# Kernel optimization log

Measured on AMD Instinct MI355X. Metric: run time of the kernel, lower is better.

The kernel has to match this reference:

```python
import jax, jax.numpy as jnp
import numpy as np

IN_FEATURES = 1024
OUT_FEATURES = 1024
BATCH = 32
SEQ = 1024
EPS = 1e-8


def setup_inputs() -> dict:
    key = jax.random.key(0)
    k1, k2, k3 = jax.random.split(key, 3)
    Efou = jax.random.normal(k1, (BATCH, SEQ, IN_FEATURES), dtype=jnp.float32)
    y = jax.random.normal(k2, (BATCH, IN_FEATURES), dtype=jnp.float32)
    weight = jax.random.normal(k3, (IN_FEATURES, OUT_FEATURES), dtype=jnp.float32)
    return {"Efou": Efou, "y": y, "weight": weight}


def reference(Efou, y, weight):
    # scale = 1/sqrt(in_features)
    scale = 1.0 / np.sqrt(np.float32(weight.shape[0]))
    ys = y * scale  # (b, i) == per-sample column scaling of weight
    # Demodulation norm: sum_i (scale*W[i,o]*y[b,i])^2 = (ys^2) @ (W^2)
    d = jax.lax.rsqrt(jnp.einsum('bi,io->bo', ys * ys, weight * weight) + EPS)  # (b, o)
    # Efou @ (scale*W*y*d) == ((Efou*ys) @ W) * d  -- same math, avoids (b,i,o) weight
    out = jnp.einsum('bsi,io->bso', Efou * ys[:, None, :], weight) * d[:, None, :]
    return out
```

## Files before the change

kernel.cpp:

```cpp
#include <hip/hip_runtime.h>

#define AS1 __attribute__((address_space(1)))
#define AS3 __attribute__((address_space(3)))

typedef __bf16 bf16x8 __attribute__((ext_vector_type(8)));
typedef float f32x4 __attribute__((ext_vector_type(4)));
typedef unsigned short ushort8 __attribute__((ext_vector_type(8)));

__device__ __forceinline__ unsigned short f2bf(float f) {
  union { float f; unsigned u; } v; v.f = f;
  unsigned u = v.u;
  unsigned r = (u + 0x7fffu + ((u >> 16) & 1u)) >> 16;
  return (unsigned short)r;
}

__global__ __launch_bounds__(256) void dcalc_a_kernel(const float* __restrict__ y,
                                                      const float* __restrict__ W,
                                                      float* __restrict__ partial) {
  __shared__ float ysq[32][32];
  const int o = blockIdx.x * 256 + threadIdx.x;
  const int i0 = blockIdx.y * 32;
  for (int e = threadIdx.x; e < 1024; e += 256) {
    int il = e >> 5, b = e & 31;
    float t = y[b * 1024 + i0 + il] * 0.03125f;
    ysq[il][b] = t * t;
  }
  __syncthreads();

  f32x4 acc[8] = {};
#pragma unroll
  for (int il = 0; il < 32; ++il) {
    float w = W[(size_t)(i0 + il) * 1024 + o];
    float w2 = w * w;
#pragma unroll
    for (int b4 = 0; b4 < 8; ++b4) {
      f32x4 q = *(const f32x4*)&ysq[il][b4 * 4];
#pragma unroll
      for (int k = 0; k < 4; ++k) acc[b4][k] = fmaf(q[k], w2, acc[b4][k]);
    }
  }
  float* p = partial + (size_t)blockIdx.y * 32768 + o;
#pragma unroll
  for (int b4 = 0; b4 < 8; ++b4)
#pragma unroll
    for (int k = 0; k < 4; ++k) p[(b4 * 4 + k) * 1024] = acc[b4][k];
}

__global__ __launch_bounds__(256) void dcalc_b_kernel(const float* __restrict__ partial,
                                                      float* __restrict__ dmod) {
  const int bo = blockIdx.x * 256 + threadIdx.x;
  float acc = 0.f;
#pragma unroll 8
  for (int is = 0; is < 32; ++is) acc += partial[(size_t)is * 32768 + bo];
  dmod[bo] = rsqrtf(acc + 1e-8f);
}

__global__ void wconv_kernel(const float* __restrict__ W,
                             unsigned short* __restrict__ WT) {
  __shared__ float t[32][33];
  const int tx = threadIdx.x;
  const int ty = threadIdx.y;
  const int i0 = blockIdx.y * 32;
  const int o0 = blockIdx.x * 32;
#pragma unroll
  for (int k = 0; k < 4; ++k)
    t[ty + k * 8][tx] = W[(size_t)(i0 + ty + k * 8) * 1024 + o0 + tx];
  __syncthreads();
#pragma unroll
  for (int k = 0; k < 4; ++k)
    WT[(size_t)(o0 + ty + k * 8) * 1024 + i0 + tx] = f2bf(t[tx][ty + k * 8]);
}

#define NT 16
#define LDS_TILE 65536

#define BAR __builtin_amdgcn_s_barrier()
#define LGKM0 asm volatile("s_waitcnt lgkmcnt(0)" ::: "memory")
#define VM(n) asm volatile("s_waitcnt vmcnt(" #n ")" ::: "memory")
#define SCHB __builtin_amdgcn_sched_barrier(0)
#define PRIO(x) __builtin_amdgcn_s_setprio(x)

#define STG_B(r, t, dst)                                                     \
  __builtin_amdgcn_global_load_lds(                                          \
      (const AS1 void*)(Ws + (size_t)(r) * 64 * 2048 + (t) * 128),           \
      (AS3 void*)((dst) + 32768 + (r) * 8192 + sldso), 16, 0, 0)

#define A_ISSUE(t)                                                           \
  {                                                                          \
    const float* asrc = Efou + (size_t)(m0 + argp * 4) * 1024 + (t) * 64 + k8; \
    _Pragma("unroll") for (int rr = 0; rr < 4; ++rr) {                       \
      pa[rr][0] = *(const f32x4*)(asrc + rr * 1024);                         \
      pa[rr][1] = *(const f32x4*)(asrc + rr * 1024 + 4);                     \
    }                                                                        \
    yv[0] = *(const f32x4*)(ysS + (t) * 64 + k8);                            \
    yv[1] = *(const f32x4*)(ysS + (t) * 64 + k8 + 4);                        \
  }

#define A_WRITE(dst)                                                         \
  {                                                                          \
    _Pragma("unroll") for (int rr = 0; rr < 4; ++rr) {                       \
      const int row = argp * 4 + rr;                                         \
      ushort8 ov;                                                            \
      _Pragma("unroll") for (int q = 0; q < 4; ++q) {                        \
        ov[q] = f2bf(pa[rr][0][q] * yv[0][q]);                               \
        ov[q + 4] = f2bf(pa[rr][1][q] * yv[1][q]);                           \
      }                                                                      \
      *(ushort8*)((dst) + row * 128 + ((kslot * 16) ^ ((row & 7) << 4))) = ov; \
    }                                                                        \
  }

#define RD_A(mh, mi, kk)                                                     \
  (*(const bf16x8*)(Ab + (wr * 128 + ((mh) * 4 + (mi)) * 16 + l15) * 128 +   \
                    ((((kk) * 64 + lhi * 16)) ^ swz_rd)))
#define RD_B(nh, ni, kk)                                                     \
  (*(const bf16x8*)(Bb + (wc * 64 + ((nh) * 2 + (ni)) * 16 + l15) * 128 +    \
                    ((((kk) * 64 + lhi * 16)) ^ swz_rd)))

#define LD_A(mh)                                                             \
  { _Pragma("unroll") for (int mi = 0; mi < 4; ++mi)                         \
      _Pragma("unroll") for (int kk = 0; kk < 2; ++kk)                       \
        a[mi][kk] = RD_A(mh, mi, kk); }
#define LD_B(nh)                                                             \
  { _Pragma("unroll") for (int ni = 0; ni < 2; ++ni)                         \
      _Pragma("unroll") for (int kk = 0; kk < 2; ++kk)                       \
        bfr[ni][kk] = RD_B(nh, ni, kk); }

#define MM(mh, nh)                                                           \
  do {                                                                       \
    _Pragma("unroll") for (int mi = 0; mi < 4; ++mi)                         \
      _Pragma("unroll") for (int ni = 0; ni < 2; ++ni)                       \
        _Pragma("unroll") for (int kk = 0; kk < 2; ++kk)                     \
          acc[(mh) * 4 + mi][(nh) * 2 + ni] =                                \
              __builtin_amdgcn_mfma_f32_16x16x32_bf16(                       \
                  a[mi][kk], bfr[ni][kk], acc[(mh) * 4 + mi][(nh) * 2 + ni], \
                  0, 0, 0);                                                  \
  } while (0)

__global__ __launch_bounds__(512, 2) void gemmf_kernel(
    const float* __restrict__ Efou, const float* __restrict__ y,
    const unsigned short* __restrict__ WT, const float* __restrict__ dmod,
    float* __restrict__ out) {
  extern __shared__ char lds[];
  float* ysS = (float*)(lds + 2 * LDS_TILE);

  const int tid = threadIdx.x;
  const int bid = blockIdx.x;
  const int wg = (bid & 7) * 64 + (bid >> 3);
  const int bm = wg >> 2, bn = wg & 3;
  const int m0 = bm * 256, n0 = bn * 256;
  const int b = m0 >> 10;

  const int w = tid >> 6, l = tid & 63;
  const int wr = w >> 2, wc = w & 3;
  const int l15 = l & 15, lhi = l >> 4;
  const int swz_rd = (l15 & 7) << 4;

  const int kslot = tid & 7;
  const int k8 = kslot * 8;
  const int argp = tid >> 3;

  const int srow = tid >> 3;
  const int scb = ((tid & 7) << 4) ^ ((srow & 7) << 4);
  const char* Ws = (const char*)WT + (size_t)(n0 + srow) * 2048 + scb;
  const int sldso = tid * 16;

  f32x4 acc[8][4] = {};
  bf16x8 a[4][2], bfr[2][2];
  f32x4 pa[4][2], yv[2];

  {
    float2 yy = *(const float2*)(y + b * 1024 + tid * 2);
    ysS[2 * tid] = yy.x * 0.03125f;
    ysS[2 * tid + 1] = yy.y * 0.03125f;
  }
  __syncthreads();
  {
    char* d0 = lds;
    STG_B(0, 0, d0); STG_B(1, 0, d0); STG_B(2, 0, d0); STG_B(3, 0, d0);
    A_ISSUE(0);
    A_WRITE(d0);
  }
  VM(0); LGKM0; BAR;

  for (int t = 0; t < NT - 1; ++t) {
    const char* Ab = lds + (t & 1) * LDS_TILE;
    const char* Bb = Ab + 32768;
    char* dN = lds + ((t & 1) ^ 1) * LDS_TILE;
    const int t1 = t + 1;
    LD_A(0); LD_B(0);
    A_ISSUE(t1);
    STG_B(0, t1, dN); STG_B(1, t1, dN);
    BAR; LGKM0; SCHB; PRIO(1); MM(0, 0); PRIO(0); SCHB; BAR;
    LD_B(1);
    STG_B(2, t1, dN); STG_B(3, t1, dN);
    BAR; LGKM0; SCHB; PRIO(1); MM(0, 1); PRIO(0); SCHB; BAR;
    LD_A(1); LD_B(0);
    BAR; LGKM0; SCHB; PRIO(1); MM(1, 0); PRIO(0); SCHB; BAR;
    LD_B(1);
    BAR; LGKM0; SCHB; PRIO(1); MM(1, 1); PRIO(0); SCHB;
    A_WRITE(dN);
    VM(0);
    LGKM0;
    BAR;
  }

  {
    const char* Ab = lds + ((NT - 1) & 1) * LDS_TILE;
    const char* Bb = Ab + 32768;
    LD_A(0); LD_B(0);
    BAR; LGKM0; SCHB; PRIO(1); MM(0, 0); PRIO(0); SCHB; BAR;
    LD_B(1);
    BAR; LGKM0; SCHB; PRIO(1); MM(0, 1); PRIO(0); SCHB; BAR;
    LD_A(1); LD_B(0);
    BAR; LGKM0; SCHB; PRIO(1); MM(1, 0); PRIO(0); SCHB; BAR;
    LD_B(1);
    BAR; LGKM0; SCHB; PRIO(1); MM(1, 1); PRIO(0); SCHB;
  }

  const int col0 = n0 + wc * 64 + l15;
  float dv[4];
#pragma unroll
  for (int nf = 0; nf < 4; ++nf) dv[nf] = dmod[b * 1024 + col0 + nf * 16];
#pragma unroll
  for (int mf = 0; mf < 8; ++mf) {
#pragma unroll
    for (int j = 0; j < 4; ++j) {
      const int row = m0 + wr * 128 + mf * 16 + lhi * 4 + j;
      float* orow = out + (size_t)row * 1024 + col0;
#pragma unroll
      for (int nf = 0; nf < 4; ++nf) orow[nf * 16] = acc[mf][nf][j] * dv[nf];
    }
  }
}

extern "C" void kernel_launch(void* const* d_in, const int* in_sizes, int n_in,
                              void* d_out, int out_size, void* d_ws, size_t ws_size,
                              hipStream_t stream) {
  const float* Efou = (const float*)d_in[0];
  const float* y    = (const float*)d_in[1];
  const float* W    = (const float*)d_in[2];
  float* out = (float*)d_out;

  unsigned short* WT = (unsigned short*)d_ws;
  float* dmod        = (float*)(WT + (size_t)1024 * 1024);
  float* dpart       = dmod + 32768;

  hipFuncSetAttribute((const void*)gemmf_kernel,
                      hipFuncAttributeMaxDynamicSharedMemorySize, 135168);

  dcalc_a_kernel<<<dim3(4, 32), 256, 0, stream>>>(y, W, dpart);
  dcalc_b_kernel<<<128, 256, 0, stream>>>(dpart, dmod);
  wconv_kernel<<<dim3(32, 32), dim3(32, 8), 0, stream>>>(W, WT);
  gemmf_kernel<<<512, 512, 135168, stream>>>(Efou, y, WT, dmod, out);
}
```

Measured before the change: 129.6 us.

## Issue A-tile loads via inline asm and convert-write mid-iteration with partial vmcnt wait

Replaces the compiler-generated fp32 A-tile global loads with inline-asm dwordx4 loads that use an SGPR base and VGPR offsets. It also moves the bf16 convert-and-LDS-write of the next A tile from the end of the iteration to the middle, after a partial vmcnt wait. All four B-stage LDS DMAs are now issued up front. The intent is to overlap the A conversion with the MFMA phases and shorten the serial tail before the barrier. The risk is that the vmcnt counts assume a fixed ordering of outstanding loads, and the LDS write now lands while MFMAs are still reading the other buffer.

Result: no change. 131.4 us (+1.4%).

```diff
diff --git a/kernel.cpp b/kernel.cpp
--- a/kernel.cpp
+++ b/kernel.cpp
@@ -85,18 +85,27 @@
       (const AS1 void*)(Ws + (size_t)(r) * 64 * 2048 + (t) * 128),           \
       (AS3 void*)((dst) + 32768 + (r) * 8192 + sldso), 16, 0, 0)
 
-#define A_ISSUE(t)                                                           \
+#define AISS(t1)                                                             \
   {                                                                          \
-    const float* asrc = Efou + (size_t)(m0 + argp * 4) * 1024 + (t) * 64 + k8; \
-    _Pragma("unroll") for (int rr = 0; rr < 4; ++rr) {                       \
-      pa[rr][0] = *(const f32x4*)(asrc + rr * 1024);                         \
-      pa[rr][1] = *(const f32x4*)(asrc + rr * 1024 + 4);                     \
-    }                                                                        \
-    yv[0] = *(const f32x4*)(ysS + (t) * 64 + k8);                            \
-    yv[1] = *(const f32x4*)(ysS + (t) * 64 + k8 + 4);                        \
-  }
-
-#define A_WRITE(dst)                                                         \
+    const unsigned _vo = avoff + (unsigned)((t1) * 256);                     \
+    asm volatile(                                                            \
+        "global_load_dwordx4 %0, %8, %12\n\t"                                \
+        "global_load_dwordx4 %1, %8, %12 offset:16\n\t"                      \
+        "global_load_dwordx4 %2, %9, %12\n\t"                                \
+        "global_load_dwordx4 %3, %9, %12 offset:16\n\t"                      \
+        "global_load_dwordx4 %4, %10, %12\n\t"                               \
+        "global_load_dwordx4 %5, %10, %12 offset:16\n\t"                     \
+        "global_load_dwordx4 %6, %11, %12\n\t"                               \
+        "global_load_dwordx4 %7, %11, %12 offset:16\n\t"                     \
+        : "=&v"(pa[0][0]), "=&v"(pa[0][1]), "=&v"(pa[1][0]),                 \
+          "=&v"(pa[1][1]), "=&v"(pa[2][0]), "=&v"(pa[2][1]),                 \
+          "=&v"(pa[3][0]), "=&v"(pa[3][1])                                   \
+        : "v"(_vo), "v"(_vo + 4096u), "v"(_vo + 8192u), "v"(_vo + 12288u),   \
+          "s"(eptr)                                                          \
+        : "memory");                                                         \
+  }
+
+#define ACVT_WR(dst)                                                         \
   {                                                                          \
     _Pragma("unroll") for (int rr = 0; rr < 4; ++rr) {                       \
       const int row = argp * 4 + rr;                                         \
@@ -136,7 +145,7 @@
                   0, 0, 0);                                                  \
   } while (0)
 
-__global__ __launch_bounds__(512, 2) void gemmf_kernel(
+__global__ __launch_bounds__(512, 2) void gemmf2_kernel(
     const float* __restrict__ Efou, const float* __restrict__ y,
     const unsigned short* __restrict__ WT, const float* __restrict__ dmod,
     float* __restrict__ out) {
@@ -158,6 +167,8 @@
   const int kslot = tid & 7;
   const int k8 = kslot * 8;
   const int argp = tid >> 3;
+  const unsigned avoff = (unsigned)((m0 + argp * 4) * 4096 + kslot * 32);
+  const unsigned long long eptr = (unsigned long long)Efou;
 
   const int srow = tid >> 3;
   const int scb = ((tid & 7) << 4) ^ ((srow & 7) << 4);
@@ -176,11 +187,16 @@
   __syncthreads();
   {
     char* d0 = lds;
+    AISS(0);
     STG_B(0, 0, d0); STG_B(1, 0, d0); STG_B(2, 0, d0); STG_B(3, 0, d0);
-    A_ISSUE(0);
-    A_WRITE(d0);
-  }
-  VM(0); LGKM0; BAR;
+    yv[0] = *(const f32x4*)(ysS + k8);
+    yv[1] = *(const f32x4*)(ysS + k8 + 4);
+    VM(4); SCHB;
+    ACVT_WR(d0);
+    VM(0);
+    LGKM0;
+    BAR;
+  }
 
   for (int t = 0; t < NT - 1; ++t) {
     const char* Ab = lds + (t & 1) * LDS_TILE;
@@ -188,19 +204,20 @@
     char* dN = lds + ((t & 1) ^ 1) * LDS_TILE;
     const int t1 = t + 1;
     LD_A(0); LD_B(0);
-    A_ISSUE(t1);
-    STG_B(0, t1, dN); STG_B(1, t1, dN);
+    yv[0] = *(const f32x4*)(ysS + t1 * 64 + k8);
+    yv[1] = *(const f32x4*)(ysS + t1 * 64 + k8 + 4);
+    AISS(t1);
+    STG_B(0, t1, dN); STG_B(1, t1, dN); STG_B(2, t1, dN); STG_B(3, t1, dN);
     BAR; LGKM0; SCHB; PRIO(1); MM(0, 0); PRIO(0); SCHB; BAR;
     LD_B(1);
-    STG_B(2, t1, dN); STG_B(3, t1, dN);
     BAR; LGKM0; SCHB; PRIO(1); MM(0, 1); PRIO(0); SCHB; BAR;
     LD_A(1); LD_B(0);
+    VM(4); SCHB;
+    ACVT_WR(dN);
     BAR; LGKM0; SCHB; PRIO(1); MM(1, 0); PRIO(0); SCHB; BAR;
     LD_B(1);
     BAR; LGKM0; SCHB; PRIO(1); MM(1, 1); PRIO(0); SCHB;
-    A_WRITE(dN);
     VM(0);
-    LGKM0;
     BAR;
   }
 
@@ -245,11 +262,11 @@
   float* dmod        = (float*)(WT + (size_t)1024 * 1024);
   float* dpart       = dmod + 32768;
 
-  hipFuncSetAttribute((const void*)gemmf_kernel,
+  hipFuncSetAttribute((const void*)gemmf2_kernel,
                       hipFuncAttributeMaxDynamicSharedMemorySize, 135168);
 
   dcalc_a_kernel<<<dim3(4, 32), 256, 0, stream>>>(y, W, dpart);
   dcalc_b_kernel<<<128, 256, 0, stream>>>(dpart, dmod);
   wconv_kernel<<<dim3(32, 32), dim3(32, 8), 0, stream>>>(W, WT);
-  gemmf_kernel<<<512, 512, 135168, stream>>>(Efou, y, WT, dmod, out);
-}
+  gemmf2_kernel<<<512, 512, 135168, stream>>>(Efou, y, WT, dmod, out);
+}
```

## Fuse weight conversion and demod reduction into prep and GEMM kernels

Applied to the files above, without the earlier changes.

Merges the bf16 transpose of W into the demodulation partial-sum kernel, so W is read only once. The final demod reduction and rsqrt move into the GEMM prologue, where the result is kept in LDS. Together these remove two launches. The A-tile convert-and-write to LDS is also moved earlier in the main loop to overlap with the MFMA phases. The trade-offs are uncoalesced-ish 16-byte WT stores, every GEMM block redundantly re-reducing 32 partials, and a stray label left in the prologue.

Result: slower. 134.3 us (+3.6%).

```diff
diff --git a/kernel.cpp b/kernel.cpp
--- a/kernel.cpp
+++ b/kernel.cpp
@@ -14,9 +14,10 @@
   return (unsigned short)r;
 }
 
-__global__ __launch_bounds__(256) void dcalc_a_kernel(const float* __restrict__ y,
-                                                      const float* __restrict__ W,
-                                                      float* __restrict__ partial) {
+__global__ __launch_bounds__(256) void prep_kernel(const float* __restrict__ y,
+                                                   const float* __restrict__ W,
+                                                   float* __restrict__ partial,
+                                                   unsigned short* __restrict__ WT) {
   __shared__ float ysq[32][32];
   const int o = blockIdx.x * 256 + threadIdx.x;
   const int i0 = blockIdx.y * 32;
@@ -28,9 +29,11 @@
   __syncthreads();
 
   f32x4 acc[8] = {};
+  ushort8 wb[4];
 #pragma unroll
   for (int il = 0; il < 32; ++il) {
     float w = W[(size_t)(i0 + il) * 1024 + o];
+    wb[il >> 3][il & 7] = f2bf(w);
     float w2 = w * w;
 #pragma unroll
     for (int b4 = 0; b4 < 8; ++b4) {
@@ -39,36 +42,14 @@
       for (int k = 0; k < 4; ++k) acc[b4][k] = fmaf(q[k], w2, acc[b4][k]);
     }
   }
+  unsigned short* wt = WT + (size_t)o * 1024 + i0;
+#pragma unroll
+  for (int q = 0; q < 4; ++q) *(ushort8*)(wt + q * 8) = wb[q];
   float* p = partial + (size_t)blockIdx.y * 32768 + o;
 #pragma unroll
   for (int b4 = 0; b4 < 8; ++b4)
 #pragma unroll
     for (int k = 0; k < 4; ++k) p[(b4 * 4 + k) * 1024] = acc[b4][k];
-}
-
-__global__ __launch_bounds__(256) void dcalc_b_kernel(const float* __restrict__ partial,
-                                                      float* __restrict__ dmod) {
-  const int bo = blockIdx.x * 256 + threadIdx.x;
-  float acc = 0.f;
-#pragma unroll 8
-  for (int is = 0; is < 32; ++is) acc += partial[(size_t)is * 32768 + bo];
-  dmod[bo] = rsqrtf(acc + 1e-8f);
-}
-
-__global__ void wconv_kernel(const float* __restrict__ W,
-                             unsigned short* __restrict__ WT) {
-  __shared__ float t[32][33];
-  const int tx = threadIdx.x;
-  const int ty = threadIdx.y;
-  const int i0 = blockIdx.y * 32;
-  const int o0 = blockIdx.x * 32;
-#pragma unroll
-  for (int k = 0; k < 4; ++k)
-    t[ty + k * 8][tx] = W[(size_t)(i0 + ty + k * 8) * 1024 + o0 + tx];
-  __syncthreads();
-#pragma unroll
-  for (int k = 0; k < 4; ++k)
-    WT[(size_t)(o0 + ty + k * 8) * 1024 + i0 + tx] = f2bf(t[tx][ty + k * 8]);
 }
 
 #define NT 16
@@ -96,7 +77,7 @@
     yv[1] = *(const f32x4*)(ysS + (t) * 64 + k8 + 4);                        \
   }
 
-#define A_WRITE(dst)                                                         \
+#define ACVT_WR(dst)                                                         \
   {                                                                          \
     _Pragma("unroll") for (int rr = 0; rr < 4; ++rr) {                       \
       const int row = argp * 4 + rr;                                         \
@@ -136,12 +117,13 @@
                   0, 0, 0);                                                  \
   } while (0)
 
-__global__ __launch_bounds__(512, 2) void gemmf_kernel(
+__global__ __launch_bounds__(512, 2) void gemmf3_kernel(
     const float* __restrict__ Efou, const float* __restrict__ y,
-    const unsigned short* __restrict__ WT, const float* __restrict__ dmod,
+    const unsigned short* __restrict__ WT, const float* __restrict__ dpart,
     float* __restrict__ out) {
   extern __shared__ char lds[];
   float* ysS = (float*)(lds + 2 * LDS_TILE);
+  float* dtab = (float*)(lds + 2 * LDS_TILE + 4096);
 
   const int tid = threadIdx.x;
   const int bid = blockIdx.x;
@@ -168,6 +150,13 @@
   bf16x8 a[4][2], bfr[2][2];
   f32x4 pa[4][2], yv[2];
 
+  if (tid < 256) {
+    const float* dp = dpart + b * 1024 + n0 + tid;
+    float s = 0.f;
+#pragma unroll 8
+    for (int is = 0; is < 32; ++is) s += dp[(size_t)is * 32768];
+    dtab[tid] = rsqrtf(s + 1e-8f);
+  }
   {
     float2 yy = *(const float2*)(y + b * 1024 + tid * 2);
     ysS[2 * tid] = yy.x * 0.03125f;
@@ -178,7 +167,8 @@
     char* d0 = lds;
     STG_B(0, 0, d0); STG_B(1, 0, d0); STG_B(2, 0, d0); STG_B(3, 0, d0);
     A_ISSUE(0);
-    A_WRITE(d0);
+    A_WRITE_PROLOGUE:
+    ACVT_WR(d0);
   }
   VM(0); LGKM0; BAR;
 
@@ -195,10 +185,10 @@
     STG_B(2, t1, dN); STG_B(3, t1, dN);
     BAR; LGKM0; SCHB; PRIO(1); MM(0, 1); PRIO(0); SCHB; BAR;
     LD_A(1); LD_B(0);
+    ACVT_WR(dN);
     BAR; LGKM0; SCHB; PRIO(1); MM(1, 0); PRIO(0); SCHB; BAR;
     LD_B(1);
     BAR; LGKM0; SCHB; PRIO(1); MM(1, 1); PRIO(0); SCHB;
-    A_WRITE(dN);
     VM(0);
     LGKM0;
     BAR;
@@ -217,16 +207,16 @@
     BAR; LGKM0; SCHB; PRIO(1); MM(1, 1); PRIO(0); SCHB;
   }
 
-  const int col0 = n0 + wc * 64 + l15;
+  const int lc0 = wc * 64 + l15;
   float dv[4];
 #pragma unroll
-  for (int nf = 0; nf < 4; ++nf) dv[nf] = dmod[b * 1024 + col0 + nf * 16];
+  for (int nf = 0; nf < 4; ++nf) dv[nf] = dtab[lc0 + nf * 16];
 #pragma unroll
   for (int mf = 0; mf < 8; ++mf) {
 #pragma unroll
     for (int j = 0; j < 4; ++j) {
       const int row = m0 + wr * 128 + mf * 16 + lhi * 4 + j;
-      float* orow = out + (size_t)row * 1024 + col0;
+      float* orow = out + (size_t)row * 1024 + n0 + lc0;
 #pragma unroll
       for (int nf = 0; nf < 4; ++nf) orow[nf * 16] = acc[mf][nf][j] * dv[nf];
     }
@@ -242,14 +232,11 @@
   float* out = (float*)d_out;
 
   unsigned short* WT = (unsigned short*)d_ws;
-  float* dmod        = (float*)(WT + (size_t)1024 * 1024);
-  float* dpart       = dmod + 32768;
-
-  hipFuncSetAttribute((const void*)gemmf_kernel,
-                      hipFuncAttributeMaxDynamicSharedMemorySize, 135168);
-
-  dcalc_a_kernel<<<dim3(4, 32), 256, 0, stream>>>(y, W, dpart);
-  dcalc_b_kernel<<<128, 256, 0, stream>>>(dpart, dmod);
-  wconv_kernel<<<dim3(32, 32), dim3(32, 8), 0, stream>>>(W, WT);
-  gemmf_kernel<<<512, 512, 135168, stream>>>(Efou, y, WT, dmod, out);
-}
+  float* dpart       = (float*)(WT + (size_t)1024 * 1024);
+
+  hipFuncSetAttribute((const void*)gemmf3_kernel,
+                      hipFuncAttributeMaxDynamicSharedMemorySize, 136192);
+
+  prep_kernel<<<dim3(4, 32), 256, 0, stream>>>(y, W, dpart, WT);
+  gemmf3_kernel<<<512, 512, 136192, stream>>>(Efou, y, WT, dpart, out);
+}
```
